# Kernel optimization log

Measured on AMD Instinct MI355X. Metric: run time of the kernel, lower is better.

## Reference

```python
import jax, jax.numpy as jnp
import numpy as np

P, F, H, OUT = 2, 64, 2, 2   # passes, inputLayerSize, heads, outputLayerSize
N, E = 50000, 400000
D_JUMP = (P + 1) * F          # 192, JumpingKnowledge 'cat' output
D_FC = D_JUMP + 1             # 193, after concat with problemType
D_HID = D_FC // 2             # 96


def setup_inputs() -> dict:
    key = jax.random.key(0)
    ks = jax.random.split(key, 20)
    s = 1.0 / np.sqrt(F)
    return {
        'x': jax.random.normal(ks[0], (N, F), dtype=jnp.float32),
        'edge_index': jax.random.randint(ks[1], (2, E), 0, N, dtype=jnp.int32),
        'edge_attr': jax.random.normal(ks[2], (E, 1), dtype=jnp.float32),
        'problemType': jax.random.normal(ks[3], (1,), dtype=jnp.float32),
        'batch': jnp.zeros((N,), dtype=jnp.int32),
        # stacked GATv2Conv params over the P layers
        'lin_l_w': jax.random.normal(ks[4], (P, F, H * F)) * s,
        'lin_l_b': jnp.zeros((P, H * F), jnp.float32),
        'lin_r_w': jax.random.normal(ks[5], (P, F, H * F)) * s,
        'lin_r_b': jnp.zeros((P, H * F), jnp.float32),
        'lin_edge_w': jax.random.normal(ks[6], (P, 1, H * F)) * s,
        'att': jax.random.normal(ks[7], (P, H, F)) * s,
        'gat_bias': jnp.zeros((P, F), jnp.float32),
        # GlobalAttention gate_nn: Linear(D_JUMP, 1) + LeakyReLU
        'gate_w': jax.random.normal(ks[8], (D_JUMP, 1)) / np.sqrt(D_JUMP),
        'gate_b': jnp.zeros((1,), jnp.float32),
        'fc1_w': jax.random.normal(ks[9], (D_FC, D_HID)) / np.sqrt(D_FC),
        'fc1_b': jnp.zeros((D_HID,), jnp.float32),
        'fc2_w': jax.random.normal(ks[10], (D_HID, D_HID)) / np.sqrt(D_HID),
        'fc2_b': jnp.zeros((D_HID,), jnp.float32),
        'fcl_w': jax.random.normal(ks[11], (D_HID, OUT)) / np.sqrt(D_HID),
        'fcl_b': jnp.zeros((OUT,), jnp.float32),
    }


def _gatv2_layer(x, src, dst, edge_attr, Wl, bl, Wr, br, We, att, bias):
    """GATv2Conv with concat=False (mean over heads), edge_dim=1."""
    n = x.shape[0]
    xl = (x @ Wl + bl).reshape(n, H, F)          # source transform
    xr = (x @ Wr + br).reshape(n, H, F)          # target transform
    ef = (edge_attr @ We).reshape(-1, H, F)      # edge transform (no bias)
    m = xl[src] + xr[dst] + ef                   # [E,H,F]
    m = jax.nn.leaky_relu(m, 0.2)
    logits = jnp.einsum('ehf,hf->eh', m, att)    # [E,H]
    # segment softmax over destination node
    lmax = jax.ops.segment_max(logits, dst, num_segments=n)
    a = jnp.exp(logits - lmax[dst])
    denom = jax.ops.segment_sum(a, dst, num_segments=n)
    alpha = a / denom[dst]                       # [E,H]
    msg = xl[src] * alpha[:, :, None]            # [E,H,F]
    out = jax.ops.segment_sum(msg, dst, num_segments=n)  # [N,H,F]
    return out.mean(axis=1) + bias               # concat=False -> head mean


def reference(x, edge_index, edge_attr, problemType, batch,
              lin_l_w, lin_l_b, lin_r_w, lin_r_b, lin_edge_w, att, gat_bias,
              gate_w, gate_b, fc1_w, fc1_b, fc2_w, fc2_b, fcl_w, fcl_b):
    src, dst = edge_index[0], edge_index[1]
    xs = [x]
    h = x
    for p in range(P):
        h = _gatv2_layer(h, src, dst, edge_attr,
                         lin_l_w[p], lin_l_b[p], lin_r_w[p], lin_r_b[p],
                         lin_edge_w[p], att[p], gat_bias[p])
        h = jax.nn.leaky_relu(h, 0.01)
        xs.append(h)
    xj = jnp.concatenate(xs, axis=1)             # JumpingKnowledge 'cat' -> [N, D_JUMP]
    # GlobalAttention pooling (single graph: batch is all zeros)
    gate = jax.nn.leaky_relu(xj @ gate_w + gate_b, 0.01)  # [N,1]
    a = jax.nn.softmax(gate, axis=0)
    pooled = jnp.sum(a * xj, axis=0, keepdims=True)       # [1, D_JUMP]
    z = jnp.concatenate([pooled.reshape(1, -1), problemType[:, None]], axis=1)  # [1, D_FC]
    z = jax.nn.leaky_relu(z @ fc1_w + fc1_b, 0.01)
    z = jax.nn.leaky_relu(z @ fc2_w + fc2_b, 0.01)
    return z @ fcl_w + fcl_b                     # [1, OUT]
```

## Files before the change

kernel.cpp:

```cpp
#include <hip/hip_runtime.h>

#define NN 50000
#define NE 400000
#define FD 64
#define NH 2
#define HF 128
#define ELLW 48
#define SCAN_NB ((NN + 255) / 256)
#define POOL_BLOCKS 512
#define NTA 64
#define GG_BLOCKS 2048

__device__ __forceinline__ float lrelu(float x, float s) { return fmaxf(x, x * s); }

__device__ __forceinline__ unsigned short f2bf(float f) {
    unsigned u = __float_as_uint(f);
    return (unsigned short)((u + 0x7FFFu + ((u >> 16) & 1u)) >> 16);
}
__device__ __forceinline__ float2 bf2f(unsigned u) {
    return make_float2(__uint_as_float(u << 16), __uint_as_float(u & 0xFFFF0000u));
}
__device__ __forceinline__ float4 bfx4(unsigned lo, unsigned hi) {
    const float2 a = bf2f(lo), b = bf2f(hi);
    return make_float4(a.x, a.y, b.x, b.y);
}

__global__ void zero_deg(int* __restrict__ deg) {
    const int i = blockIdx.x * 256 + threadIdx.x;
    if (i < NN) deg[i] = 0;
}

__global__ void build_ell(const int* __restrict__ ei, const float* __restrict__ ea,
                          int* __restrict__ deg, int2* __restrict__ ell) {
    const int t = blockIdx.x * blockDim.x + threadIdx.x;
    if (t >= NE) return;
    const int d = ei[NE + t];
    const int r = atomicAdd(&deg[d], 1);
    ell[(size_t)d * ELLW + r] = make_int2(ei[t], __float_as_int(ea[t]));
}

__global__ __launch_bounds__(256) void node_transform(
    const float* __restrict__ hin,
    const float* __restrict__ Wl, const float* __restrict__ bl,
    const float* __restrict__ Wr, const float* __restrict__ br,
    unsigned short* __restrict__ xlb, unsigned short* __restrict__ xrb) {
    __shared__ float sA[FD][68];
    const int t = threadIdx.x;
    const int n0 = blockIdx.x * NTA;
    for (int idx = t; idx < NTA * 16; idx += 256) {
        const int n = idx & 63;
        const int kq = (idx >> 6) << 2;
        const int ni = n0 + n;
        const float4 v = (ni < NN) ? *(const float4*)(hin + (size_t)ni * FD + kq)
                                   : make_float4(0.f, 0.f, 0.f, 0.f);
        sA[kq][n] = v.x; sA[kq + 1][n] = v.y;
        sA[kq + 2][n] = v.z; sA[kq + 3][n] = v.w;
    }
    __syncthreads();
    const int q = t & 63;
    const int g = t >> 6;
    const int c0 = q << 2;
    const bool isR = c0 >= 128;
    const int cc = isR ? c0 - 128 : c0;
    const float* __restrict__ W = isR ? Wr : Wl;
    const float4 bv = isR ? *(const float4*)(br + cc) : *(const float4*)(bl + cc);
    unsigned short* __restrict__ dst = isR ? xrb : xlb;
    float acc[16][4];
#pragma unroll
    for (int i = 0; i < 16; ++i) {
        acc[i][0] = bv.x; acc[i][1] = bv.y; acc[i][2] = bv.z; acc[i][3] = bv.w;
    }
    const int nb = g << 4;
#pragma unroll 4
    for (int k = 0; k < FD; ++k) {
        const float4 w = *(const float4*)(W + k * HF + cc);
        const float4 a0 = *(const float4*)(&sA[k][nb]);
        const float4 a1 = *(const float4*)(&sA[k][nb + 4]);
        const float4 a2 = *(const float4*)(&sA[k][nb + 8]);
        const float4 a3 = *(const float4*)(&sA[k][nb + 12]);
        const float av[16] = {a0.x, a0.y, a0.z, a0.w, a1.x, a1.y, a1.z, a1.w,
                              a2.x, a2.y, a2.z, a2.w, a3.x, a3.y, a3.z, a3.w};
#pragma unroll
        for (int i = 0; i < 16; ++i) {
            acc[i][0] = fmaf(av[i], w.x, acc[i][0]);
            acc[i][1] = fmaf(av[i], w.y, acc[i][1]);
            acc[i][2] = fmaf(av[i], w.z, acc[i][2]);
            acc[i][3] = fmaf(av[i], w.w, acc[i][3]);
        }
    }
    const int xoff = (cc < 64) ? (cc << 1) : (((cc - 64) << 1) + 4);
#pragma unroll
    for (int i = 0; i < 16; ++i) {
        const int n = n0 + nb + i;
        if (n >= NN) continue;
        uint2 pk;
        pk.x = (unsigned)f2bf(acc[i][0]) | ((unsigned)f2bf(acc[i][1]) << 16);
        pk.y = (unsigned)f2bf(acc[i][2]) | ((unsigned)f2bf(acc[i][3]) << 16);
        *(uint2*)(dst + (size_t)n * HF + xoff) = pk;
    }
}

__device__ __forceinline__ void gat_edge(
    bool valid, int lane, float eav, uint4 L,
    const float4& we0, const float4& we1, const float4& aw0, const float4& aw1,
    const float4& xr0, const float4& xr1,
    float4& a0, float4& a1, float& d0, float& d1) {
    const float4 xls0 = bfx4(L.x, L.y);
    const float4 xls1 = bfx4(L.z, L.w);
    float p0, p1, t;
    t = lrelu(fmaf(eav, we0.x, xls0.x + xr0.x), 0.2f); p0 = t * aw0.x;
    t = lrelu(fmaf(eav, we0.y, xls0.y + xr0.y), 0.2f); p0 = fmaf(t, aw0.y, p0);
    t = lrelu(fmaf(eav, we0.z, xls0.z + xr0.z), 0.2f); p0 = fmaf(t, aw0.z, p0);
    t = lrelu(fmaf(eav, we0.w, xls0.w + xr0.w), 0.2f); p0 = fmaf(t, aw0.w, p0);
    t = lrelu(fmaf(eav, we1.x, xls1.x + xr1.x), 0.2f); p1 = t * aw1.x;
    t = lrelu(fmaf(eav, we1.y, xls1.y + xr1.y), 0.2f); p1 = fmaf(t, aw1.y, p1);
    t = lrelu(fmaf(eav, we1.z, xls1.z + xr1.z), 0.2f); p1 = fmaf(t, aw1.z, p1);
    t = lrelu(fmaf(eav, we1.w, xls1.w + xr1.w), 0.2f); p1 = fmaf(t, aw1.w, p1);
    const bool hi = (lane & 8) != 0;
    float send = hi ? p0 : p1;
    float got = __shfl_xor(send, 8);
    float q = hi ? (p1 + got) : (p0 + got);
    q += __shfl_xor(q, 4);
    q += __shfl_xor(q, 2);
    q += __shfl_xor(q, 1);
    const float oth = __shfl_xor(q, 8);
    const float s0 = hi ? oth : q;
    const float s1 = hi ? q : oth;
    const float w0 = valid ? __expf(s0) : 0.f;
    const float w1 = valid ? __expf(s1) : 0.f;
    a0.x = fmaf(w0, xls0.x, a0.x);
    a0.y = fmaf(w0, xls0.y, a0.y);
    a0.z = fmaf(w0, xls0.z, a0.z);
    a0.w = fmaf(w0, xls0.w, a0.w);
    d0 += w0;
    a1.x = fmaf(w1, xls1.x, a1.x);
    a1.y = fmaf(w1, xls1.y, a1.y);
    a1.z = fmaf(w1, xls1.z, a1.z);
    a1.w = fmaf(w1, xls1.w, a1.w);
    d1 += w1;
}

__global__ __launch_bounds__(256) void gat_gather(
    const int* __restrict__ deg, const int2* __restrict__ ell,
    const unsigned short* __restrict__ xlb, const unsigned short* __restrict__ xrb,
    const float* __restrict__ We, const float* __restrict__ att,
    const float* __restrict__ bias, float* __restrict__ hout) {
    const int t = threadIdx.x;
    const int lane = t & 63;
    const int slot = lane >> 4;
    const int fo = (lane & 15) << 2;
    const float4 we0 = *(const float4*)(We + fo);
    const float4 we1 = *(const float4*)(We + 64 + fo);
    const float4 aw0 = *(const float4*)(att + fo);
    const float4 aw1 = *(const float4*)(att + 64 + fo);
    const float4 bv = *(const float4*)(bias + fo);
    const int stride = (GG_BLOCKS * 256) >> 6;
    int wid = (blockIdx.x * 256 + t) >> 6;
    int dg = 0;
    int2 pA = make_int2(0, 0), pB = make_int2(0, 0);
    if (wid < NN) {
        dg = deg[wid];
        pA = ell[(size_t)wid * ELLW + slot];
        pB = ell[(size_t)wid * ELLW + 4 + slot];
    }

    while (wid < NN) {
        const int nxt = wid + stride;
        int dgn = 0;
        int2 nA = make_int2(0, 0), nB = make_int2(0, 0);
        if (nxt < NN) {
            dgn = deg[nxt];
            nA = ell[(size_t)nxt * ELLW + slot];
            nB = ell[(size_t)nxt * ELLW + 4 + slot];
        }
        const uint4 xrp = *(const uint4*)(xrb + (size_t)wid * HF + (fo << 1));
        const float4 xr0 = bfx4(xrp.x, xrp.y);
        const float4 xr1 = bfx4(xrp.z, xrp.w);
        const int e0 = wid * ELLW;
        const int e1 = e0 + dg;
        float d0 = 0.f, d1 = 0.f;
        float4 a0 = {0.f, 0.f, 0.f, 0.f}, a1 = {0.f, 0.f, 0.f, 0.f};
        {
            const bool vA = slot < dg, vB = 4 + slot < dg;
            const int sA = vA ? pA.x : 0;
            const int sB = vB ? pB.x : 0;
            const uint4 LA = *(const uint4*)(xlb + (size_t)sA * HF + (fo << 1));
            const uint4 LB = *(const uint4*)(xlb + (size_t)sB * HF + (fo << 1));
            gat_edge(vA, lane, __int_as_float(pA.y), LA, we0, we1, aw0, aw1,
                     xr0, xr1, a0, a1, d0, d1);
            gat_edge(vB, lane, __int_as_float(pB.y), LB, we0, we1, aw0, aw1,
                     xr0, xr1, a0, a1, d0, d1);
        }
        int eb = e0 + 8;
        for (; eb + 8 <= e1; eb += 8) {
            const int2 seA = ell[eb + slot];
            const int2 seB = ell[eb + 4 + slot];
            const uint4 LA = *(const uint4*)(xlb + (size_t)seA.x * HF + (fo << 1));
            const uint4 LB = *(const uint4*)(xlb + (size_t)seB.x * HF + (fo << 1));
            gat_edge(true, lane, __int_as_float(seA.y), LA, we0, we1, aw0, aw1,
                     xr0, xr1, a0, a1, d0, d1);
            gat_edge(true, lane, __int_as_float(seB.y), LB, we0, we1, aw0, aw1,
                     xr0, xr1, a0, a1, d0, d1);
        }
        if (eb < e1) {
            const int myA = eb + slot, myB = eb + 4 + slot;
            const bool vA = myA < e1, vB = myB < e1;
            const int2 seA = ell[vA ? myA : e0];
            const int2 seB = ell[vB ? myB : e0];
            const uint4 LA = *(const uint4*)(xlb + (size_t)seA.x * HF + (fo << 1));
            const uint4 LB = *(const uint4*)(xlb + (size_t)seB.x * HF + (fo << 1));
            gat_edge(vA, lane, __int_as_float(seA.y), LA, we0, we1, aw0, aw1,
                     xr0, xr1, a0, a1, d0, d1);
            gat_edge(vB, lane, __int_as_float(seB.y), LB, we0, we1, aw0, aw1,
                     xr0, xr1, a0, a1, d0, d1);
        }
#pragma unroll
        for (int o = 16; o <= 32; o <<= 1) {
            d0 += __shfl_xor(d0, o);
            d1 += __shfl_xor(d1, o);
            a0.x += __shfl_xor(a0.x, o); a0.y += __shfl_xor(a0.y, o);
            a0.z += __shfl_xor(a0.z, o); a0.w += __shfl_xor(a0.w, o);
            a1.x += __shfl_xor(a1.x, o); a1.y += __shfl_xor(a1.y, o);
            a1.z += __shfl_xor(a1.z, o); a1.w += __shfl_xor(a1.w, o);
        }
        if (slot == 0) {
            const float i0 = d0 > 0.f ? 1.f / d0 : 0.f;
            const float i1 = d1 > 0.f ? 1.f / d1 : 0.f;
            float4 rr;
            rr.x = lrelu(fmaf(0.5f, fmaf(a0.x, i0, a1.x * i1), bv.x), 0.01f);
            rr.y = lrelu(fmaf(0.5f, fmaf(a0.y, i0, a1.y * i1), bv.y), 0.01f);
            rr.z = lrelu(fmaf(0.5f, fmaf(a0.z, i0, a1.z * i1), bv.z), 0.01f);
            rr.w = lrelu(fmaf(0.5f, fmaf(a0.w, i0, a1.w * i1), bv.w), 0.01f);
            *(float4*)(hout + (size_t)wid * FD + fo) = rr;
        }
        wid = nxt;
        dg = dgn;
        pA = nA;
        pB = nB;
    }
}

__global__ void pool_kernel(const float* __restrict__ x, const float* __restrict__ h1,
                            const float* __restrict__ h2, const float* __restrict__ gw,
                            const float* __restrict__ gb, float* __restrict__ part) {
    __shared__ float sp[193];
    const int t = threadIdx.x;
    if (t < 193) sp[t] = 0.f;
    __syncthreads();
    const int lane = t & 63;
    const int wid = (blockIdx.x * blockDim.x + t) >> 6;
    const int nw = (POOL_BLOCKS * 256) >> 6;
    const float w0 = gw[lane], w1 = gw[64 + lane], w2 = gw[128 + lane];
    const float gbv = gb[0];
    float p0 = 0.f, p1 = 0.f, p2 = 0.f, es = 0.f;
    for (int n = wid; n < NN; n += nw) {
        const size_t b = (size_t)n * FD + lane;
        const float xv = x[b], h1v = h1[b], h2v = h2[b];
        float v = xv * w0 + h1v * w1 + h2v * w2;
#pragma unroll
        for (int o = 32; o; o >>= 1) v += __shfl_xor(v, o);
        const float e = __expf(lrelu(v + gbv, 0.01f));
        p0 = fmaf(e, xv, p0);
        p1 = fmaf(e, h1v, p1);
        p2 = fmaf(e, h2v, p2);
        es += e;
    }
    atomicAdd(&sp[lane], p0);
    atomicAdd(&sp[64 + lane], p1);
    atomicAdd(&sp[128 + lane], p2);
    if (lane == 0) atomicAdd(&sp[192], es);
    __syncthreads();
    if (t < 193) part[(size_t)t * POOL_BLOCKS + blockIdx.x] = sp[t];
}

__global__ void pool_reduce(const float* __restrict__ part, float* __restrict__ pooled) {
    __shared__ float ws[4];
    const int e = blockIdx.x;
    const int t = threadIdx.x;
    float s = 0.f;
#pragma unroll
    for (int b = t; b < POOL_BLOCKS; b += 256) s += part[(size_t)e * POOL_BLOCKS + b];
#pragma unroll
    for (int o = 32; o; o >>= 1) s += __shfl_xor(s, o);
    if ((t & 63) == 0) ws[t >> 6] = s;
    __syncthreads();
    if (t == 0) pooled[e] = ws[0] + ws[1] + ws[2] + ws[3];
}

__global__ void mlp_kernel(const float* __restrict__ pooled, const float* __restrict__ pt,
                           const float* __restrict__ f1w, const float* __restrict__ f1b,
                           const float* __restrict__ f2w, const float* __restrict__ f2b,
                           const float* __restrict__ flw, const float* __restrict__ flb,
                           float* __restrict__ out) {
    __shared__ float z[193], z1[96], z2[96];
    const int t = threadIdx.x;
    const float inv = 1.f / pooled[192];
    for (int i = t; i < 192; i += 256) z[i] = pooled[i] * inv;
    if (t == 0) z[192] = pt[0];
    __syncthreads();
    if (t < 96) {
        float a = f1b[t];
        for (int k = 0; k < 193; ++k) a = fmaf(z[k], f1w[k * 96 + t], a);
        z1[t] = lrelu(a, 0.01f);
    }
    __syncthreads();
    if (t < 96) {
        float a = f2b[t];
        for (int k = 0; k < 96; ++k) a = fmaf(z1[k], f2w[k * 96 + t], a);
        z2[t] = lrelu(a, 0.01f);
    }
    __syncthreads();
    if (t < 2) {
        float a = flb[t];
        for (int k = 0; k < 96; ++k) a = fmaf(z2[k], flw[k * 2 + t], a);
        out[t] = a;
    }
}

extern "C" void kernel_launch(void* const* d_in, const int* in_sizes, int n_in,
                              void* d_out, int out_size, void* d_ws, size_t ws_size,
                              hipStream_t stream) {
    (void)in_sizes; (void)n_in; (void)out_size; (void)ws_size;
    const float* x    = (const float*)d_in[0];
    const int*   ei   = (const int*)d_in[1];
    const float* ea   = (const float*)d_in[2];
    const float* pt   = (const float*)d_in[3];
    const float* llw  = (const float*)d_in[5];
    const float* llb  = (const float*)d_in[6];
    const float* lrw  = (const float*)d_in[7];
    const float* lrb  = (const float*)d_in[8];
    const float* lew  = (const float*)d_in[9];
    const float* attw = (const float*)d_in[10];
    const float* gbias= (const float*)d_in[11];
    const float* gw   = (const float*)d_in[12];
    const float* gb   = (const float*)d_in[13];
    const float* f1w  = (const float*)d_in[14];
    const float* f1b  = (const float*)d_in[15];
    const float* f2w  = (const float*)d_in[16];
    const float* f2b  = (const float*)d_in[17];
    const float* flw  = (const float*)d_in[18];
    const float* flb  = (const float*)d_in[19];
    float* out = (float*)d_out;

    char* w = (char*)d_ws;
    unsigned short* xlb = (unsigned short*)w; w += (size_t)NN * HF * 2;
    unsigned short* xrb = (unsigned short*)w; w += (size_t)NN * HF * 2;
    float* h1 = (float*)w;         w += (size_t)NN * FD * 4;
    float* h2 = (float*)w;         w += (size_t)NN * FD * 4;
    int2* ell = (int2*)w;          w += (size_t)NN * ELLW * 8;
    int* deg = (int*)w;            w += (size_t)NN * 4;
    float* part = (float*)w;       w += (size_t)193 * POOL_BLOCKS * 4;
    float* pooled = (float*)w;     w += 193 * 4;

    zero_deg<<<SCAN_NB, 256, 0, stream>>>(deg);
    build_ell<<<(NE + 255) / 256, 256, 0, stream>>>(ei, ea, deg, ell);

    for (int p = 0; p < 2; ++p) {
        const float* hin = (p == 0) ? x : h1;
        float* hout = (p == 0) ? h1 : h2;
        node_transform<<<(NN + NTA - 1) / NTA, 256, 0, stream>>>(
            hin, llw + (size_t)p * FD * HF, llb + (size_t)p * HF,
            lrw + (size_t)p * FD * HF, lrb + (size_t)p * HF, xlb, xrb);
        gat_gather<<<GG_BLOCKS, 256, 0, stream>>>(
            deg, ell, xlb, xrb,
            lew + (size_t)p * HF, attw + (size_t)p * HF,
            gbias + (size_t)p * FD, hout);
    }

    pool_kernel<<<POOL_BLOCKS, 256, 0, stream>>>(x, h1, h2, gw, gb, part);
    pool_reduce<<<193, 256, 0, stream>>>(part, pooled);
    mlp_kernel<<<1, 256, 0, stream>>>(pooled, pt, f1w, f1b, f2w, f2b, flw, flb, out);
}
```

Baseline: 197.5 us.

## Compute node transform with bf16 MFMA instead of FP32 FMA loops

```diff
diff --git a/kernel.cpp b/kernel.cpp
--- a/kernel.cpp
+++ b/kernel.cpp
@@ -8,8 +8,10 @@
 #define ELLW 48
 #define SCAN_NB ((NN + 255) / 256)
 #define POOL_BLOCKS 512
-#define NTA 64
 #define GG_BLOCKS 2048
+
+typedef __attribute__((ext_vector_type(8))) short bf16x8;
+typedef __attribute__((ext_vector_type(4))) float f32x4;
 
 __device__ __forceinline__ float lrelu(float x, float s) { return fmaxf(x, x * s); }
 
@@ -44,59 +46,53 @@
     const float* __restrict__ Wl, const float* __restrict__ bl,
     const float* __restrict__ Wr, const float* __restrict__ br,
     unsigned short* __restrict__ xlb, unsigned short* __restrict__ xrb) {
-    __shared__ float sA[FD][68];
-    const int t = threadIdx.x;
-    const int n0 = blockIdx.x * NTA;
-    for (int idx = t; idx < NTA * 16; idx += 256) {
-        const int n = idx & 63;
-        const int kq = (idx >> 6) << 2;
-        const int ni = n0 + n;
-        const float4 v = (ni < NN) ? *(const float4*)(hin + (size_t)ni * FD + kq)
-                                   : make_float4(0.f, 0.f, 0.f, 0.f);
-        sA[kq][n] = v.x; sA[kq + 1][n] = v.y;
-        sA[kq + 2][n] = v.z; sA[kq + 3][n] = v.w;
-    }
-    __syncthreads();
-    const int q = t & 63;
-    const int g = t >> 6;
-    const int c0 = q << 2;
-    const bool isR = c0 >= 128;
-    const int cc = isR ? c0 - 128 : c0;
-    const float* __restrict__ W = isR ? Wr : Wl;
-    const float4 bv = isR ? *(const float4*)(br + cc) : *(const float4*)(bl + cc);
-    unsigned short* __restrict__ dst = isR ? xrb : xlb;
-    float acc[16][4];
-#pragma unroll
-    for (int i = 0; i < 16; ++i) {
-        acc[i][0] = bv.x; acc[i][1] = bv.y; acc[i][2] = bv.z; acc[i][3] = bv.w;
-    }
-    const int nb = g << 4;
+    __shared__ unsigned short Ab[64][72];
+    __shared__ unsigned short Bb[256][72];
+    const int t = threadIdx.x;
+    const int n0b = blockIdx.x * 64;
+    for (int idx = t; idx < 64 * 16; idx += 256) {
+        const int m = idx >> 4, kq = (idx & 15) << 2;
+        const int node = n0b + m;
+        const float4 v = (node < NN) ? *(const float4*)(hin + (size_t)node * FD + kq)
+                                     : make_float4(0.f, 0.f, 0.f, 0.f);
+        Ab[m][kq] = f2bf(v.x); Ab[m][kq + 1] = f2bf(v.y);
+        Ab[m][kq + 2] = f2bf(v.z); Ab[m][kq + 3] = f2bf(v.w);
+    }
+    for (int idx = t; idx < 64 * 64; idx += 256) {
+        const int k = idx >> 6;
+        const int cq = idx & 63;
+        const int c4 = (cq & 31) << 2;
+        const float4 v = (cq < 32) ? *(const float4*)(Wl + k * HF + c4)
+                                   : *(const float4*)(Wr + k * HF + c4);
+        const int n = ((cq < 32) ? 0 : 128) + c4;
+        Bb[n][k] = f2bf(v.x); Bb[n + 1][k] = f2bf(v.y);
+        Bb[n + 2][k] = f2bf(v.z); Bb[n + 3][k] = f2bf(v.w);
+    }
+    __syncthreads();
+    const int wv = t >> 6, lane = t & 63;
+    const int m0 = wv << 4;
+    const int lr = lane & 15, lg = lane >> 4;
+    const bf16x8 af0 = *(const bf16x8*)(&Ab[m0 + lr][lg * 8]);
+    const bf16x8 af1 = *(const bf16x8*)(&Ab[m0 + lr][32 + lg * 8]);
 #pragma unroll 4
-    for (int k = 0; k < FD; ++k) {
-        const float4 w = *(const float4*)(W + k * HF + cc);
-        const float4 a0 = *(const float4*)(&sA[k][nb]);
-        const float4 a1 = *(const float4*)(&sA[k][nb + 4]);
-        const float4 a2 = *(const float4*)(&sA[k][nb + 8]);
-        const float4 a3 = *(const float4*)(&sA[k][nb + 12]);
-        const float av[16] = {a0.x, a0.y, a0.z, a0.w, a1.x, a1.y, a1.z, a1.w,
-                              a2.x, a2.y, a2.z, a2.w, a3.x, a3.y, a3.z, a3.w};
-#pragma unroll
-        for (int i = 0; i < 16; ++i) {
-            acc[i][0] = fmaf(av[i], w.x, acc[i][0]);
-            acc[i][1] = fmaf(av[i], w.y, acc[i][1]);
-            acc[i][2] = fmaf(av[i], w.z, acc[i][2]);
-            acc[i][3] = fmaf(av[i], w.w, acc[i][3]);
-        }
-    }
-    const int xoff = (cc < 64) ? (cc << 1) : (((cc - 64) << 1) + 4);
-#pragma unroll
-    for (int i = 0; i < 16; ++i) {
-        const int n = n0 + nb + i;
-        if (n >= NN) continue;
-        uint2 pk;
-        pk.x = (unsigned)f2bf(acc[i][0]) | ((unsigned)f2bf(acc[i][1]) << 16);
-        pk.y = (unsigned)f2bf(acc[i][2]) | ((unsigned)f2bf(acc[i][3]) << 16);
-        *(uint2*)(dst + (size_t)n * HF + xoff) = pk;
+    for (int nt = 0; nt < 16; ++nt) {
+        const int c = (nt << 4) + lr;
+        const bf16x8 bf0 = *(const bf16x8*)(&Bb[c][lg * 8]);
+        const bf16x8 bf1 = *(const bf16x8*)(&Bb[c][32 + lg * 8]);
+        f32x4 acc = {0.f, 0.f, 0.f, 0.f};
+        acc = __builtin_amdgcn_mfma_f32_16x16x32_bf16(af0, bf0, acc, 0, 0, 0);
+        acc = __builtin_amdgcn_mfma_f32_16x16x32_bf16(af1, bf1, acc, 0, 0, 0);
+        const bool isR = c >= 128;
+        const int cc = isR ? c - 128 : c;
+        const float bv = isR ? br[cc] : bl[cc];
+        unsigned short* __restrict__ dst = isR ? xrb : xlb;
+        const int pos = (cc < 64) ? (((cc >> 2) << 3) + (cc & 3))
+                                  : ((((cc - 64) >> 2) << 3) + 4 + (cc & 3));
+#pragma unroll
+        for (int r = 0; r < 4; ++r) {
+            const int node = n0b + m0 + lg * 4 + r;
+            if (node < NN) dst[(size_t)node * HF + pos] = f2bf(acc[r] + bv);
+        }
     }
 }
 
@@ -358,7 +354,7 @@
     for (int p = 0; p < 2; ++p) {
         const float* hin = (p == 0) ? x : h1;
         float* hout = (p == 0) ? h1 : h2;
-        node_transform<<<(NN + NTA - 1) / NTA, 256, 0, stream>>>(
+        node_transform<<<(NN + 63) / 64, 256, 0, stream>>>(
             hin, llw + (size_t)p * FD * HF, llb + (size_t)p * HF,
             lrw + (size_t)p * FD * HF, lrb + (size_t)p * HF, xlb, xrb);
         gat_gather<<<GG_BLOCKS, 256, 0, stream>>>(
```

Result: slower. 207.3 us (+5.0%).
